# Performance work log

Measured on AMD Instinct MI355X. Metric: run time of the kernel, lower is better.

## Reference

```python
import jax, jax.numpy as jnp
import numpy as np

NUM_TYPES = 8
NUM_TAGS = 1 + 2 * NUM_TYPES  # tag 0 = 'O', 2t+1 = 'B-t', 2t+2 = 'I-t'
NEG = -10000.0


def _bio_constraints(num_types):
    K = 1 + 2 * num_types
    allowed = np.zeros((K, K), dtype=np.float32)
    for i in range(K):
        for j in range(K):
            if j == 0 or (j % 2 == 1):  # to O or to B-y: always allowed
                allowed[i, j] = 1.0
            else:  # to I-y: only from B-y or I-y
                y = (j - 2) // 2
                if i in (2 * y + 1, 2 * y + 2):
                    allowed[i, j] = 1.0
    start = np.array([1.0 if (j == 0 or j % 2 == 1) else 0.0 for j in range(K)], dtype=np.float32)
    end = np.ones((K,), dtype=np.float32)  # BIO: any tag may end a sequence
    return allowed, start, end


def setup_inputs() -> dict:
    key = jax.random.key(0)
    ks = jax.random.split(key, 8)
    B, T, D, K = 64, 512, 1024, NUM_TAGS
    mlm_out = jax.random.normal(ks[0], (B, T, D), dtype=jnp.float32)
    lengths = jax.random.randint(ks[1], (B,), T // 4, T + 1)  # variable lengths >= 1
    mask = (jnp.arange(T)[None, :] < lengths[:, None])  # bool [B,T], left-padded-free
    gold = jax.random.randint(ks[2], (B, T), 0, K)
    W = jax.random.normal(ks[3], (D, K), dtype=jnp.float32) * 0.02
    b = jnp.zeros((K,), dtype=jnp.float32)
    transitions = jax.random.normal(ks[4], (K, K), dtype=jnp.float32) * 0.1
    start_trans = jax.random.normal(ks[5], (K,), dtype=jnp.float32) * 0.1
    end_trans = jax.random.normal(ks[6], (K,), dtype=jnp.float32) * 0.1
    ta, sa, ea = _bio_constraints(NUM_TYPES)
    return {"mlm_out": mlm_out, "mask": mask, "gold": gold, "W": W, "b": b,
            "transitions": transitions, "start_trans": start_trans, "end_trans": end_trans,
            "trans_allowed": jnp.asarray(ta), "start_allowed": jnp.asarray(sa), "end_allowed": jnp.asarray(ea)}


def reference(mlm_out, mask, gold, W, b, transitions, start_trans, end_trans,
              trans_allowed, start_allowed, end_allowed):
    logits = jnp.einsum('btd,dk->btk', mlm_out, W) + b  # [B,T,K]
    maskf = mask.astype(logits.dtype)
    B, T, K = logits.shape

    # ---- joint (numerator) score, AllenNLP semantics ----
    score = start_trans[gold[:, 0]]
    pair = transitions[gold[:, :-1], gold[:, 1:]]                       # [B,T-1]
    emit = jnp.take_along_axis(logits, gold[:, :, None], axis=2)[..., 0]  # [B,T]
    score = score + jnp.sum(pair * maskf[:, 1:], axis=1) + jnp.sum(emit[:, :-1] * maskf[:, :-1], axis=1)
    lengths = jnp.sum(mask.astype(jnp.int32), axis=1)
    last_tags = jnp.take_along_axis(gold, (lengths - 1)[:, None], axis=1)[:, 0]
    last_emit = jnp.take_along_axis(logits[:, -1, :], last_tags[:, None], axis=1)[:, 0]
    score = score + end_trans[last_tags] + last_emit * maskf[:, -1]

    # ---- partition function (forward algorithm, log-space scan over time) ----
    logits_t = jnp.swapaxes(logits, 0, 1)  # [T,B,K]
    mask_t = jnp.swapaxes(maskf, 0, 1)     # [T,B]
    alpha0 = start_trans + logits_t[0]

    def fstep(alpha, xs):
        emit_t, m = xs
        inner = alpha[:, :, None] + transitions[None] + emit_t[:, None, :]  # [B,K,K]
        new = jax.scipy.special.logsumexp(inner, axis=1)
        return jnp.where(m[:, None] > 0, new, alpha), None

    alphaT, _ = jax.lax.scan(fstep, alpha0, (logits_t[1:], mask_t[1:]))
    logZ = jax.scipy.special.logsumexp(alphaT + end_trans, axis=1)

    loss = -jnp.sum(score - logZ)  # loss_weight = 1.0

    # ---- Viterbi decode with BIO-constrained transitions ----
    ct = transitions * trans_allowed + NEG * (1.0 - trans_allowed)
    cs = start_trans * start_allowed + NEG * (1.0 - start_allowed)
    ce = end_trans * end_allowed + NEG * (1.0 - end_allowed)
    v0 = cs + logits_t[0]

    def vstep(v, xs):
        emit_t, m = xs
        inner = v[:, :, None] + ct[None]          # [B,K,K]
        bp = jnp.argmax(inner, axis=1)            # [B,K] best prev tag per next tag
        best = jnp.max(inner, axis=1) + emit_t
        return jnp.where(m[:, None] > 0, best, v), bp

    vT, bps = jax.lax.scan(vstep, v0, (logits_t[1:], mask_t[1:]))  # bps [T-1,B,K]
    last_tag = jnp.argmax(vT + ce, axis=1)  # [B]

    def btstep(tag, xs):
        bp, m = xs
        prev = jnp.take_along_axis(bp, tag[:, None], axis=1)[:, 0]
        prev = jnp.where(m > 0, prev, tag)  # padded steps: carry tag through
        return prev, tag

    first_tag, tags_rest = jax.lax.scan(btstep, last_tag, (bps, mask_t[1:]), reverse=True)
    pred = jnp.concatenate([first_tag[None], tags_rest], axis=0).swapaxes(0, 1)  # [B,T]
    pred = pred * mask.astype(pred.dtype)
    return logits, loss, pred
```

## Files before the change

kernel.cpp:

```cpp
#include <hip/hip_runtime.h>
#include <math.h>

#define KK 17
#define TT 512
#define DD 1024
#define NBATCH 64
#define NEGC -10000.0f
#define NINF -1e30f
#define EMS 516

__device__ __forceinline__ float wsum64(float v) {
#pragma unroll
  for (int s = 32; s >= 1; s >>= 1) v += __shfl_xor(v, s);
  return v;
}
__device__ __forceinline__ int wsum64i(int v) {
#pragma unroll
  for (int s = 32; s >= 1; s >>= 1) v += __shfl_xor(v, s);
  return v;
}
__device__ __forceinline__ float rl(float x, int i) {
  return __int_as_float(__builtin_amdgcn_readlane(__float_as_int(x), i));
}

__global__ __launch_bounds__(512) void k_logits(const float* __restrict__ X,
                                                const float* __restrict__ W,
                                                const float* __restrict__ b,
                                                float* __restrict__ logits) {
  __shared__ float Ws[512 * KK];
  const int tid = threadIdx.x;
  const int lane = tid & 63;
  const int wv = tid >> 6;
  const long r0 = (long)blockIdx.x * 32 + wv * 4;
  const float* x0 = X + r0 * DD;
  float a0[KK], a1[KK], a2[KK], a3[KK];
#pragma unroll
  for (int j = 0; j < KK; ++j) { a0[j] = 0.f; a1[j] = 0.f; a2[j] = 0.f; a3[j] = 0.f; }

  for (int half = 0; half < 2; ++half) {
    __syncthreads();
#pragma unroll
    for (int i = 0; i < KK; ++i) {
      int idx = tid + i * 512;
      Ws[idx] = W[half * 512 * KK + idx];
    }
    __syncthreads();
#pragma unroll
    for (int it = 0; it < 8; ++it) {
      int k = it * 64 + lane;
      float xa = x0[half * 512 + k];
      float xb = x0[DD + half * 512 + k];
      float xc = x0[2 * DD + half * 512 + k];
      float xd = x0[3 * DD + half * 512 + k];
#pragma unroll
      for (int j = 0; j < KK; ++j) {
        float w = Ws[k * KK + j];
        a0[j] = fmaf(xa, w, a0[j]);
        a1[j] = fmaf(xb, w, a1[j]);
        a2[j] = fmaf(xc, w, a2[j]);
        a3[j] = fmaf(xd, w, a3[j]);
      }
    }
  }
#pragma unroll
  for (int j = 0; j < KK; ++j) {
    a0[j] = wsum64(a0[j]); a1[j] = wsum64(a1[j]);
    a2[j] = wsum64(a2[j]); a3[j] = wsum64(a3[j]);
  }
  if (lane < KK) {
    float v0 = 0.f, v1 = 0.f, v2 = 0.f, v3 = 0.f;
#pragma unroll
    for (int j = 0; j < KK; ++j)
      if (lane == j) { v0 = a0[j]; v1 = a1[j]; v2 = a2[j]; v3 = a3[j]; }
    float bb = b[lane];
    logits[r0 * KK + lane] = v0 + bb;
    logits[(r0 + 1) * KK + lane] = v1 + bb;
    logits[(r0 + 2) * KK + lane] = v2 + bb;
    logits[(r0 + 3) * KK + lane] = v3 + bb;
  }
}

#define ARGM(vl, il, vr, ir, vo, io) \
  { bool tk = (vr) > (vl); vo = tk ? (vr) : (vl); io = tk ? (ir) : (il); }

__global__ __launch_bounds__(256) void k_scan(
    const float* __restrict__ logits, const void* __restrict__ maskp,
    const int* __restrict__ gold, const float* __restrict__ trans,
    const float* __restrict__ st, const float* __restrict__ et,
    const float* __restrict__ ta, const float* __restrict__ sa,
    const float* __restrict__ ea, float* __restrict__ lossp,
    float* __restrict__ predp) {
  __shared__ __align__(16) float EMT[KK * EMS];
  __shared__ __align__(4) unsigned char Mk[512];
  __shared__ unsigned char BPt[511 * KK];
  __shared__ unsigned char G2t[256 * KK];
  __shared__ unsigned char G4t[128 * KK];
  __shared__ unsigned char G8t[64 * KK];
  __shared__ unsigned char PR[512];
  __shared__ float red[2];
  __shared__ int shlt;

  const int tid = threadIdx.x;
  const int lane = tid & 63;
  const int wv = tid >> 6;
  const int batch = blockIdx.x;
  const float* Lg = logits + (size_t)batch * TT * KK;

  const unsigned char* mb = (const unsigned char*)maskp;
  const bool m_is_i32 = (mb[1] == 0);

  {
    const float4* Lg4 = reinterpret_cast<const float4*>(Lg);
    for (int i = tid; i < (TT * KK) / 4; i += 256) {
      float4 v = Lg4[i];
      int n = i * 4;
      int t0 = n / KK, j0 = n - t0 * KK;
      float vv[4] = {v.x, v.y, v.z, v.w};
#pragma unroll
      for (int e = 0; e < 4; ++e) {
        int j = j0 + e, t = t0;
        if (j >= KK) { j -= KK; t += 1; }
        EMT[j * EMS + t] = vv[e];
      }
    }
    if (m_is_i32) {
      const int* mi = (const int*)maskp + batch * TT;
      for (int t2 = tid; t2 < TT; t2 += 256) Mk[t2] = (unsigned char)(mi[t2] != 0);
    } else {
      const unsigned char* mB = mb + batch * TT;
      for (int t2 = tid; t2 < TT; t2 += 256) Mk[t2] = (unsigned char)(mB[t2] != 0);
    }
  }
  __syncthreads();
  int len;
  {
    const unsigned int* Mku = reinterpret_cast<const unsigned int*>(Mk);
    unsigned int a = Mku[lane], b2 = Mku[64 + lane];
    int c = (int)(((a * 0x01010101u) >> 24) + ((b2 * 0x01010101u) >> 24));
    len = wsum64i(c);
  }

  const int jc = lane < KK ? lane : (KK - 1);
  const float* EMTrow = EMT + jc * EMS;

  if (wv == 0) {
    float ctv[KK];
#pragma unroll
    for (int i = 0; i < KK; ++i)
      ctv[i] = (ta[i * KK + jc] > 0.5f) ? trans[i * KK + jc] : NEGC;
    unsigned char* bpw = BPt + jc;
    const bool act = lane < KK;
    float4 A = *reinterpret_cast<const float4*>(EMTrow);
    float v = ((sa[jc] > 0.5f) ? st[jc] : NEGC) + A.x;
    int t = 1;

#define VSTEP(EMV)                                                        \
    {                                                                     \
      float c0 = rl(v, 0) + ctv[0], c1 = rl(v, 1) + ctv[1];               \
      float c2 = rl(v, 2) + ctv[2], c3 = rl(v, 3) + ctv[3];               \
      float c4 = rl(v, 4) + ctv[4], c5 = rl(v, 5) + ctv[5];               \
      float c6 = rl(v, 6) + ctv[6], c7 = rl(v, 7) + ctv[7];               \
      float c8 = rl(v, 8) + ctv[8], c9 = rl(v, 9) + ctv[9];               \
      float c10 = rl(v, 10) + ctv[10], c11 = rl(v, 11) + ctv[11];         \
      float c12 = rl(v, 12) + ctv[12], c13 = rl(v, 13) + ctv[13];         \
      float c14 = rl(v, 14) + ctv[14], c15 = rl(v, 15) + ctv[15];         \
      float c16 = rl(v, 16) + ctv[16];                                    \
      float d0, d1, d2, d3, d4, d5, d6, d7;                               \
      int j0, j1, j2, j3, j4, j5, j6, j7;                                 \
      ARGM(c0, 0, c1, 1, d0, j0) ARGM(c2, 2, c3, 3, d1, j1)               \
      ARGM(c4, 4, c5, 5, d2, j2) ARGM(c6, 6, c7, 7, d3, j3)               \
      ARGM(c8, 8, c9, 9, d4, j4) ARGM(c10, 10, c11, 11, d5, j5)           \
      ARGM(c12, 12, c13, 13, d6, j6) ARGM(c14, 14, c15, 15, d7, j7)       \
      float e0, e1, e2, e3; int k0, k1, k2, k3;                           \
      ARGM(d0, j0, d1, j1, e0, k0) ARGM(d2, j2, d3, j3, e1, k1)           \
      ARGM(d4, j4, d5, j5, e2, k2) ARGM(d6, j6, d7, j7, e3, k3)           \
      float f0, f1; int l0, l1;                                           \
      ARGM(e0, k0, e1, k1, f0, l0) ARGM(e2, k2, e3, k3, f1, l1)           \
      float g0; int m0i;                                                  \
      ARGM(f0, l0, f1, l1, g0, m0i)                                       \
      float bv; int bi;                                                   \
      ARGM(g0, m0i, c16, 16, bv, bi)                                      \
      if (act) bpw[0] = (unsigned char)bi;                                \
      bpw += KK;                                                          \
      float vn = bv + (EMV);                                              \
      v = (t < len) ? vn : v;                                             \
      ++t;                                                                \
    }

    for (int g = 0; g < 127; ++g) {
      float4 B = *reinterpret_cast<const float4*>(EMTrow + 4 * g + 4);
      VSTEP(A.y) VSTEP(A.z) VSTEP(A.w) VSTEP(B.x)
      A = B;
    }
    VSTEP(A.y) VSTEP(A.z) VSTEP(A.w)
#undef VSTEP

    float fv = v + ((ea[jc] > 0.5f) ? et[jc] : NEGC);
    float best = rl(fv, 0);
    int bidx = 0;
#pragma unroll
    for (int i = 1; i < KK; ++i) {
      float fi = rl(fv, i);
      bool tk = fi > best;
      best = tk ? fi : best;
      bidx = tk ? i : bidx;
    }
    if (tid == 0) shlt = bidx;
  } else if (wv == 1) {
    float Pcol[KK];
#pragma unroll
    for (int i = 0; i < KK; ++i) Pcol[i] = __expf(trans[i * KK + jc]);
    float4 A = *reinterpret_cast<const float4*>(EMTrow);
    float a0v = st[jc] + A.x;
    float m0 = rl(a0v, 0);
#pragma unroll
    for (int i = 1; i < KK; ++i) m0 = fmaxf(m0, rl(a0v, i));
    float qown = __expf(a0v - m0);
    float C = m0;
    float ee = __expf(A.y);
    int t = 1;

#define FSTEP(EMNEXT, DOREN)                                                   \
    {                                                                          \
      float q0 = rl(qown, 0), q1 = rl(qown, 1), q2 = rl(qown, 2);              \
      float q3 = rl(qown, 3), q4 = rl(qown, 4), q5 = rl(qown, 5);              \
      float q6 = rl(qown, 6), q7 = rl(qown, 7), q8 = rl(qown, 8);              \
      float q9 = rl(qown, 9), q10 = rl(qown, 10), q11 = rl(qown, 11);          \
      float q12 = rl(qown, 12), q13 = rl(qown, 13), q14 = rl(qown, 14);        \
      float q15 = rl(qown, 15), q16 = rl(qown, 16);                            \
      float da = fmaf(q0, Pcol[0], fmaf(q4, Pcol[4], fmaf(q8, Pcol[8],         \
                 fmaf(q12, Pcol[12], q16 * Pcol[16]))));                       \
      float db = fmaf(q1, Pcol[1], fmaf(q5, Pcol[5], fmaf(q9, Pcol[9],         \
                 q13 * Pcol[13])));                                            \
      float dc = fmaf(q2, Pcol[2], fmaf(q6, Pcol[6], fmaf(q10, Pcol[10],       \
                 q14 * Pcol[14])));                                            \
      float dd = fmaf(q3, Pcol[3], fmaf(q7, Pcol[7], fmaf(q11, Pcol[11],       \
                 q15 * Pcol[15])));                                            \
      float qn = ((da + db) + (dc + dd)) * ee;                                 \
      ee = __expf(EMNEXT);                                                     \
      float qs = (t < len) ? qn : qown;                                        \
      if (DOREN) {                                                             \
        float s0 = ((q0 + q1) + (q2 + q3)) + ((q4 + q5) + (q6 + q7));          \
        float s1 = ((q8 + q9) + (q10 + q11)) + ((q12 + q13) + (q14 + q15));    \
        float s = (s0 + s1) + q16;                                             \
        C += __logf(s);                                                        \
        qs *= (1.0f / s);                                                      \
      }                                                                        \
      qown = qs;                                                               \
      ++t;                                                                     \
    }

    for (int g = 0; g < 127; ++g) {
      float4 B = *reinterpret_cast<const float4*>(EMTrow + 4 * g + 4);
      FSTEP(A.z, false) FSTEP(A.w, false) FSTEP(B.x, false)
      FSTEP(B.y, (g & 1))
      A = B;
    }
    FSTEP(A.z, false) FSTEP(A.w, false) FSTEP(A.w, false)
#undef FSTEP

    float term = qown * __expf(et[jc]);
    float S = rl(term, 0);
#pragma unroll
    for (int i = 1; i < KK; ++i) S += rl(term, i);
    if (lane == 0) red[0] = C + __logf(S);
  } else if (wv == 2) {
    const int* gb = gold + batch * TT;
    float esum = 0.f, tsum = 0.f;
#pragma unroll
    for (int u = 0; u < 8; ++u) {
      int t = lane + 64 * u;
      int gt = gb[t];
      float mt = (float)Mk[t];
      esum += mt * EMT[gt * EMS + t];
      int tn = (t + 1 < TT) ? t + 1 : TT - 1;
      int gn = gb[tn];
      float mtr = (t + 1 < TT && Mk[t + 1]) ? 1.f : 0.f;
      tsum += mtr * trans[gt * KK + gn];
    }
    float ssum = wsum64(esum + tsum);
    if (lane == 0) red[1] = ssum + st[gb[0]] + et[gb[len - 1]];
  }
  __syncthreads();
  if (tid == 0) atomicAdd(lossp, red[0] - red[1]);

  const int lt = shlt;
  {
    int m = tid;
    int s1 = 2 * m + 1, s0b = 2 * m;
    bool u1 = (s1 < 511) && Mk[s1 + 1];
    bool u0 = Mk[s0b + 1] != 0;
#pragma unroll
    for (int x = 0; x < KK; ++x) {
      int y = u1 ? (int)BPt[s1 * KK + x] : x;
      int z = u0 ? (int)BPt[s0b * KK + y] : y;
      G2t[m * KK + x] = (unsigned char)z;
    }
  }
  __syncthreads();
  if (tid < 128) {
    int p = tid;
#pragma unroll
    for (int x = 0; x < KK; ++x) {
      int y = G2t[(2 * p + 1) * KK + x];
      G4t[p * KK + x] = G2t[2 * p * KK + y];
    }
  }
  __syncthreads();
  if (tid < 64) {
    int p = tid;
#pragma unroll
    for (int x = 0; x < KK; ++x) {
      int y = G4t[(2 * p + 1) * KK + x];
      G8t[p * KK + x] = G4t[2 * p * KK + y];
    }
  }
  __syncthreads();
  if (tid == 0) {
    int x = lt;
    for (int p = 63; p >= 0; --p) {
      x = G8t[p * KK + x];
      PR[8 * p] = (unsigned char)x;
    }
  }
  __syncthreads();
  if (tid < 64) {
    int p = tid;
    int src = (p == 63) ? lt : (int)PR[8 * p + 8];
    PR[8 * p + 4] = G4t[(2 * p + 1) * KK + src];
  }
  __syncthreads();
  if (tid < 128) {
    int m = tid;
    int src = (m == 127) ? lt : (int)PR[4 * m + 4];
    PR[4 * m + 2] = G2t[(2 * m + 1) * KK + src];
  }
  __syncthreads();
  {
    int m = tid;
    int s = 2 * m + 1;
    int src = (m == 255) ? lt : (int)PR[2 * m + 2];
    int val = ((s < 511) && Mk[s + 1]) ? (int)BPt[s * KK + src] : src;
    PR[2 * m + 1] = (unsigned char)val;
  }
  __syncthreads();
  float* po = predp + batch * TT;
  for (int t2 = tid; t2 < TT; t2 += 256) po[t2] = Mk[t2] ? (float)PR[t2] : 0.f;
}

extern "C" void kernel_launch(void* const* d_in, const int* in_sizes, int n_in,
                              void* d_out, int out_size, void* d_ws, size_t ws_size,
                              hipStream_t stream) {
  const float* mlm = (const float*)d_in[0];
  const void* mask = d_in[1];
  const int* gold = (const int*)d_in[2];
  const float* W = (const float*)d_in[3];
  const float* b = (const float*)d_in[4];
  const float* trans = (const float*)d_in[5];
  const float* st = (const float*)d_in[6];
  const float* et = (const float*)d_in[7];
  const float* ta = (const float*)d_in[8];
  const float* sa = (const float*)d_in[9];
  const float* ea = (const float*)d_in[10];

  float* out = (float*)d_out;
  float* logits = out;
  float* lossp = out + (size_t)NBATCH * TT * KK;
  float* predp = lossp + 1;

  hipMemsetAsync(lossp, 0, sizeof(float), stream);
  k_logits<<<dim3(1024), dim3(512), 0, stream>>>(mlm, W, b, logits);
  k_scan<<<dim3(64), dim3(256), 0, stream>>>(logits, mask, gold, trans, st, et,
                                             ta, sa, ea, lossp, predp);
}
```

Measured before the change: 375.7 us.

## Vectorize logits GEMV, use DPP reductions, max3 Viterbi step, drop memset

The logits kernel now stores W transposed in shared memory and reads X and W as float4, cutting load instruction count. Its cross-lane reduction uses DPP row operations plus a readlane instead of xor shuffles. In the Viterbi scan, the pairwise argmax tree becomes a v_max3 tree followed by an equality scan that recovers the lowest matching index, which shortens the dependent chain on the serial critical path. The loss zeroing moves from a separate memset into the first block of the logits kernel, removing one launch; this relies on the scan kernel running after the logits kernel on the same stream.

Result: no change. 375.8 us (+0.0%).

```diff
diff --git a/kernel.cpp b/kernel.cpp
--- a/kernel.cpp
+++ b/kernel.cpp
@@ -8,6 +8,7 @@
 #define NEGC -10000.0f
 #define NINF -1e30f
 #define EMS 516
+#define WTS 520
 
 __device__ __forceinline__ float wsum64(float v) {
 #pragma unroll
@@ -22,15 +23,29 @@
 __device__ __forceinline__ float rl(float x, int i) {
   return __int_as_float(__builtin_amdgcn_readlane(__float_as_int(x), i));
 }
+__device__ __forceinline__ float dppsum(float v) {
+  float t;
+  t = __int_as_float(__builtin_amdgcn_update_dpp(0, __float_as_int(v), 0x111, 0xf, 0xf, true));  v += t;
+  t = __int_as_float(__builtin_amdgcn_update_dpp(0, __float_as_int(v), 0x112, 0xf, 0xf, true));  v += t;
+  t = __int_as_float(__builtin_amdgcn_update_dpp(0, __float_as_int(v), 0x114, 0xf, 0xf, true));  v += t;
+  t = __int_as_float(__builtin_amdgcn_update_dpp(0, __float_as_int(v), 0x118, 0xf, 0xf, true));  v += t;
+  t = __int_as_float(__builtin_amdgcn_update_dpp(0, __float_as_int(v), 0x142, 0xa, 0xf, false)); v += t;
+  t = __int_as_float(__builtin_amdgcn_update_dpp(0, __float_as_int(v), 0x143, 0xc, 0xf, false)); v += t;
+  return v;
+}
+#define MAX3(d, a, b, c) \
+  asm("v_max3_f32 %0, %1, %2, %3" : "=v"(d) : "v"(a), "v"(b), "v"(c));
 
 __global__ __launch_bounds__(512) void k_logits(const float* __restrict__ X,
                                                 const float* __restrict__ W,
                                                 const float* __restrict__ b,
-                                                float* __restrict__ logits) {
-  __shared__ float Ws[512 * KK];
+                                                float* __restrict__ logits,
+                                                float* __restrict__ lossp) {
+  __shared__ __align__(16) float Wt[KK * WTS];
   const int tid = threadIdx.x;
   const int lane = tid & 63;
   const int wv = tid >> 6;
+  if (blockIdx.x == 0 && tid == 0) *lossp = 0.f;
   const long r0 = (long)blockIdx.x * 32 + wv * 4;
   const float* x0 = X + r0 * DD;
   float a0[KK], a1[KK], a2[KK], a3[KK];
@@ -39,39 +54,46 @@
 
   for (int half = 0; half < 2; ++half) {
     __syncthreads();
-#pragma unroll
-    for (int i = 0; i < KK; ++i) {
-      int idx = tid + i * 512;
-      Ws[idx] = W[half * 512 * KK + idx];
+    {
+      const float* wr = W + (size_t)(half * 512 + tid) * KK;
+#pragma unroll
+      for (int j = 0; j < KK; ++j) Wt[j * WTS + tid] = wr[j];
     }
     __syncthreads();
 #pragma unroll
-    for (int it = 0; it < 8; ++it) {
-      int k = it * 64 + lane;
-      float xa = x0[half * 512 + k];
-      float xb = x0[DD + half * 512 + k];
-      float xc = x0[2 * DD + half * 512 + k];
-      float xd = x0[3 * DD + half * 512 + k];
+    for (int it = 0; it < 2; ++it) {
+      const int k4 = it * 256 + lane * 4;
+      const float* xp = x0 + half * 512 + k4;
+      float4 xa = *reinterpret_cast<const float4*>(xp);
+      float4 xb = *reinterpret_cast<const float4*>(xp + DD);
+      float4 xc = *reinterpret_cast<const float4*>(xp + 2 * DD);
+      float4 xd = *reinterpret_cast<const float4*>(xp + 3 * DD);
 #pragma unroll
       for (int j = 0; j < KK; ++j) {
-        float w = Ws[k * KK + j];
-        a0[j] = fmaf(xa, w, a0[j]);
-        a1[j] = fmaf(xb, w, a1[j]);
-        a2[j] = fmaf(xc, w, a2[j]);
-        a3[j] = fmaf(xd, w, a3[j]);
+        float4 w = *reinterpret_cast<const float4*>(&Wt[j * WTS + k4]);
+        a0[j] = fmaf(xa.x, w.x, a0[j]); a0[j] = fmaf(xa.y, w.y, a0[j]);
+        a0[j] = fmaf(xa.z, w.z, a0[j]); a0[j] = fmaf(xa.w, w.w, a0[j]);
+        a1[j] = fmaf(xb.x, w.x, a1[j]); a1[j] = fmaf(xb.y, w.y, a1[j]);
+        a1[j] = fmaf(xb.z, w.z, a1[j]); a1[j] = fmaf(xb.w, w.w, a1[j]);
+        a2[j] = fmaf(xc.x, w.x, a2[j]); a2[j] = fmaf(xc.y, w.y, a2[j]);
+        a2[j] = fmaf(xc.z, w.z, a2[j]); a2[j] = fmaf(xc.w, w.w, a2[j]);
+        a3[j] = fmaf(xd.x, w.x, a3[j]); a3[j] = fmaf(xd.y, w.y, a3[j]);
+        a3[j] = fmaf(xd.z, w.z, a3[j]); a3[j] = fmaf(xd.w, w.w, a3[j]);
       }
     }
   }
 #pragma unroll
   for (int j = 0; j < KK; ++j) {
-    a0[j] = wsum64(a0[j]); a1[j] = wsum64(a1[j]);
-    a2[j] = wsum64(a2[j]); a3[j] = wsum64(a3[j]);
+    a0[j] = dppsum(a0[j]); a1[j] = dppsum(a1[j]);
+    a2[j] = dppsum(a2[j]); a3[j] = dppsum(a3[j]);
+  }
+  float v0 = 0.f, v1 = 0.f, v2 = 0.f, v3 = 0.f;
+#pragma unroll
+  for (int j = 0; j < KK; ++j) {
+    float s0 = rl(a0[j], 63), s1 = rl(a1[j], 63), s2 = rl(a2[j], 63), s3 = rl(a3[j], 63);
+    if (lane == j) { v0 = s0; v1 = s1; v2 = s2; v3 = s3; }
   }
   if (lane < KK) {
-    float v0 = 0.f, v1 = 0.f, v2 = 0.f, v3 = 0.f;
-#pragma unroll
-    for (int j = 0; j < KK; ++j)
-      if (lane == j) { v0 = a0[j]; v1 = a1[j]; v2 = a2[j]; v3 = a3[j]; }
     float bb = b[lane];
     logits[r0 * KK + lane] = v0 + bb;
     logits[(r0 + 1) * KK + lane] = v1 + bb;
@@ -79,9 +101,6 @@
     logits[(r0 + 3) * KK + lane] = v3 + bb;
   }
 }
-
-#define ARGM(vl, il, vr, ir, vo, io) \
-  { bool tk = (vr) > (vl); vo = tk ? (vr) : (vl); io = tk ? (ir) : (il); }
 
 __global__ __launch_bounds__(256) void k_scan(
     const float* __restrict__ logits, const void* __restrict__ maskp,
@@ -165,25 +184,25 @@
       float c12 = rl(v, 12) + ctv[12], c13 = rl(v, 13) + ctv[13];         \
       float c14 = rl(v, 14) + ctv[14], c15 = rl(v, 15) + ctv[15];         \
       float c16 = rl(v, 16) + ctv[16];                                    \
-      float d0, d1, d2, d3, d4, d5, d6, d7;                               \
-      int j0, j1, j2, j3, j4, j5, j6, j7;                                 \
-      ARGM(c0, 0, c1, 1, d0, j0) ARGM(c2, 2, c3, 3, d1, j1)               \
-      ARGM(c4, 4, c5, 5, d2, j2) ARGM(c6, 6, c7, 7, d3, j3)               \
-      ARGM(c8, 8, c9, 9, d4, j4) ARGM(c10, 10, c11, 11, d5, j5)           \
-      ARGM(c12, 12, c13, 13, d6, j6) ARGM(c14, 14, c15, 15, d7, j7)       \
-      float e0, e1, e2, e3; int k0, k1, k2, k3;                           \
-      ARGM(d0, j0, d1, j1, e0, k0) ARGM(d2, j2, d3, j3, e1, k1)           \
-      ARGM(d4, j4, d5, j5, e2, k2) ARGM(d6, j6, d7, j7, e3, k3)           \
-      float f0, f1; int l0, l1;                                           \
-      ARGM(e0, k0, e1, k1, f0, l0) ARGM(e2, k2, e3, k3, f1, l1)           \
-      float g0; int m0i;                                                  \
-      ARGM(f0, l0, f1, l1, g0, m0i)                                       \
-      float bv; int bi;                                                   \
-      ARGM(g0, m0i, c16, 16, bv, bi)                                      \
+      float x0, x1, x2, x3, x4, y0, y1, bv;                               \
+      MAX3(x0, c0, c1, c2)   MAX3(x1, c3, c4, c5)                         \
+      MAX3(x2, c6, c7, c8)   MAX3(x3, c9, c10, c11)                       \
+      MAX3(x4, c12, c13, c14)                                             \
+      MAX3(y0, x0, x1, x2)   MAX3(y1, x3, x4, c15)                        \
+      MAX3(bv, y0, y1, c16)                                               \
+      float vn = bv + (EMV);                                              \
+      v = (t < len) ? vn : v;                                             \
+      int bi = 16;                                                        \
+      bi = (c15 == bv) ? 15 : bi; bi = (c14 == bv) ? 14 : bi;             \
+      bi = (c13 == bv) ? 13 : bi; bi = (c12 == bv) ? 12 : bi;             \
+      bi = (c11 == bv) ? 11 : bi; bi = (c10 == bv) ? 10 : bi;             \
+      bi = (c9 == bv) ? 9 : bi;   bi = (c8 == bv) ? 8 : bi;               \
+      bi = (c7 == bv) ? 7 : bi;   bi = (c6 == bv) ? 6 : bi;               \
+      bi = (c5 == bv) ? 5 : bi;   bi = (c4 == bv) ? 4 : bi;               \
+      bi = (c3 == bv) ? 3 : bi;   bi = (c2 == bv) ? 2 : bi;               \
+      bi = (c1 == bv) ? 1 : bi;   bi = (c0 == bv) ? 0 : bi;               \
       if (act) bpw[0] = (unsigned char)bi;                                \
       bpw += KK;                                                          \
-      float vn = bv + (EMV);                                              \
-      v = (t < len) ? vn : v;                                             \
       ++t;                                                                \
     }
 
@@ -368,8 +387,7 @@
   float* lossp = out + (size_t)NBATCH * TT * KK;
   float* predp = lossp + 1;
 
-  hipMemsetAsync(lossp, 0, sizeof(float), stream);
-  k_logits<<<dim3(1024), dim3(512), 0, stream>>>(mlm, W, b, logits);
+  k_logits<<<dim3(1024), dim3(512), 0, stream>>>(mlm, W, b, logits, lossp);
   k_scan<<<dim3(64), dim3(256), 0, stream>>>(logits, mask, gold, trans, st, et,
                                              ta, sa, ea, lossp, predp);
 }
```
